# Optimization experiments

Hardware: AMD Instinct MI355X
Metric: run time of the kernel (lower is better)

The kernel has to match this reference:

```python
import jax, jax.numpy as jnp
import numpy as np

K = 8  # K_num: neighbors per pred point


def setup_inputs() -> dict:
    key = jax.random.key(0)
    ks = jax.random.split(key, 8)
    B, Nr, Np, C = 2, 8192, 8192, 256
    s = 1.0 / np.sqrt(C)
    return {
        "xyz_ref": jax.random.normal(ks[0], (B, Nr, 3), jnp.float32) * 10.0,
        "xyz_pred": jax.random.normal(ks[1], (B, Np, 3), jnp.float32) * 10.0,
        "feat_k_ref": jax.random.normal(ks[2], (B, Nr, C), jnp.float32),
        "feat_q_pred": jax.random.normal(ks[3], (B, Np, C), jnp.float32),
        "feat_v_ref": jax.random.normal(ks[4], (B, Nr, C), jnp.float32),
        "Wv": jax.random.normal(ks[5], (C, C), jnp.float32) * s,
        "bv": jnp.zeros((C,), jnp.float32),
        "Wo": jax.random.normal(ks[6], (C, C), jnp.float32) * s,
        "bo": jnp.zeros((C,), jnp.float32),
        "Wout": jax.random.normal(ks[7], (2 * C, C), jnp.float32) * s,
    }


def reference(xyz_ref, xyz_pred, feat_k_ref, feat_q_pred, feat_v_ref, Wv, bv, Wo, bo, Wout):
    B, Np, C = feat_q_pred.shape
    Nr = feat_k_ref.shape[1]

    # --- KNN search (torch.no_grad in original) ---
    xr = jax.lax.stop_gradient(xyz_ref)
    xp = jax.lax.stop_gradient(xyz_pred)
    d2 = (jnp.sum(xp * xp, -1)[:, :, None]
          + jnp.sum(xr * xr, -1)[:, None, :]
          - 2.0 * jnp.einsum('bpd,brd->bpr', xp, xr))  # [B, Np, Nr]
    _, idx = jax.lax.top_k(-d2, K)  # [B, Np, K] nearest ref indices per pred point

    # --- W_v (Conv1d 1x1) applied to all ref values before gather ---
    v_all = jnp.einsum('brc,dc->brd', feat_v_ref, Wv) + bv  # [B, Nr, C]

    gather = jax.vmap(lambda f, i: f[i])  # per-sample fancy gather
    k = gather(feat_k_ref, idx)  # [B, Np, K, C]
    v = gather(v_all, idx)       # [B, Np, K, C]

    # --- tiny per-point cross attention over K neighbors ---
    scores = jnp.einsum('bpc,bpkc->bpk', feat_q_pred, k) / jnp.sqrt(jnp.asarray(C, feat_q_pred.dtype))
    attn = jax.nn.softmax(scores, axis=-1)          # [B, Np, K]
    out = jnp.einsum('bpk,bpkc->bpc', attn, v)      # [B, Np, C]

    # --- W_o (Conv1d 1x1) ---
    out = jnp.einsum('bpc,dc->bpd', out, Wo) + bo   # [B, Np, C]

    # --- scatter into full point set: ref rows stay zero, pred rows get out ---
    out_all = jnp.concatenate([jnp.zeros((B, Nr, C), out.dtype), out], axis=1)  # [B, Nr+Np, C]

    # --- W_out (MinkowskiConvolution k=1, no bias): C -> 2C ---
    return jnp.einsum('bnc,dc->bnd', out_all, Wout)  # [B, Nr+Np, 2C]
```

## Files before the change

kernel.cpp:

```cpp
#include <hip/hip_runtime.h>
#include <stdint.h>


#define NRr 8192
#define NPp 8192
#define NC  256
#define NK  8
#define NCH   16
#define CHUNK 512

typedef short bf16x8 __attribute__((ext_vector_type(8)));
typedef float f32x4  __attribute__((ext_vector_type(4)));

__device__ __forceinline__ uint16_t f2bf(float f) {
  uint32_t u = __float_as_uint(f);
  return (uint16_t)((u + 0x7fffu + ((u >> 16) & 1u)) >> 16);
}

__device__ __forceinline__ float d2f(float px, float py, float pz, float sp, float4 r) {
  float m0 = __fmul_rn(px, r.x), m1 = __fmul_rn(py, r.y), m2 = __fmul_rn(pz, r.z);
  float dot = __fadd_rn(__fadd_rn(m0, m1), m2);
  return __fsub_rn(__fadd_rn(sp, r.w), __fadd_rn(dot, dot));
}

__device__ __forceinline__ uint32_t fkey(float f) {
  uint32_t b = __float_as_uint(f);
  return (b & 0x80000000u) ? ~b : (b | 0x80000000u);
}

__global__ __launch_bounds__(64) void k_prep(const float* __restrict__ xyz_ref,
                                             float4* __restrict__ ref4) {
  int i = blockIdx.x * 64 + threadIdx.x;
  if (i >= 2 * NRr) return;
  float x = xyz_ref[i*3+0];
  float y = xyz_ref[i*3+1];
  float z = xyz_ref[i*3+2];
  float n = __fadd_rn(__fadd_rn(__fmul_rn(x,x), __fmul_rn(y,y)), __fmul_rn(z,z));
  ref4[i] = make_float4(x, y, z, n);
}

__device__ __forceinline__ void insert8(float d2, int j, float (&dist)[8], int (&id)[8]) {
  if (d2 < dist[7]) {
    #pragma unroll
    for (int k = 7; k >= 1; --k) {
      bool sh = d2 < dist[k-1];
      bool pl = d2 < dist[k];
      float nd = sh ? dist[k-1] : (pl ? d2 : dist[k]);
      int   ni = sh ? id[k-1]   : (pl ? j  : id[k]);
      dist[k] = nd; id[k] = ni;
    }
    if (d2 < dist[0]) { dist[0] = d2; id[0] = j; }
  }
}

__global__ __launch_bounds__(256, 5) void k_knn(const float* __restrict__ xyz_pred,
                                                const float4* __restrict__ ref4,
                                                uint16_t* __restrict__ part,
                                                const float* __restrict__ Wv,
                                                const float* __restrict__ bv,
                                                const float* __restrict__ Wo,
                                                const float* __restrict__ bo,
                                                const float* __restrict__ Wout,
                                                uint16_t* __restrict__ Aw,
                                                float* __restrict__ bbig) {
  __shared__ __align__(16) char smem[32768];

  if (blockIdx.x < 64) {
    float (*M8)[256] = (float (*)[256])smem;
    float* red = (float*)(smem + 8192);
    int e0 = blockIdx.x * 8;
    int t  = threadIdx.x;

    float acc8[8];
    #pragma unroll
    for (int e = 0; e < 8; ++e) acc8[e] = 0.f;
    for (int d = 0; d < 256; ++d) {
      float wo = Wo[(size_t)d*256 + t];
      #pragma unroll
      for (int e = 0; e < 8; ++e)
        acc8[e] = fmaf(Wout[(size_t)(e0+e)*256 + d], wo, acc8[e]);
    }
    #pragma unroll
    for (int e = 0; e < 8; ++e) M8[e][t] = acc8[e];
    __syncthreads();

    float a8[8];
    #pragma unroll
    for (int e = 0; e < 8; ++e) a8[e] = 0.f;
    for (int c = 0; c < 256; ++c) {
      float wv = Wv[(size_t)c*256 + t];
      #pragma unroll
      for (int e = 0; e < 8; ++e)
        a8[e] = fmaf(M8[e][c], wv, a8[e]);
    }
    #pragma unroll
    for (int e = 0; e < 8; ++e) Aw[(size_t)(e0+e)*256 + t] = f2bf(a8[e]);

    for (int e = 0; e < 8; ++e) {
      red[t] = fmaf(M8[e][t], bv[t], Wout[(size_t)(e0+e)*256 + t] * bo[t]);
      __syncthreads();
      for (int s2 = 128; s2 > 0; s2 >>= 1) {
        if (t < s2) red[t] += red[t + s2];
        __syncthreads();
      }
      if (t == 0) bbig[e0+e] = red[0];
      __syncthreads();
    }
    return;
  }

  float4* sref = (float4*)smem;
  int wave = threadIdx.x >> 6;
  int lane = threadIdx.x & 63;
  int task = (blockIdx.x - 64) * 4 + wave;
  int ch   = task & (NCH - 1);
  int P    = (task >> 4) * 64 + lane;
  int b    = P >> 13;

  float px = xyz_pred[P*3+0];
  float py = xyz_pred[P*3+1];
  float pz = xyz_pred[P*3+2];
  float sp = __fadd_rn(__fadd_rn(__fmul_rn(px,px), __fmul_rn(py,py)), __fmul_rn(pz,pz));

  const float4* refbase = ref4 + (size_t)b * NRr;
  int rbase = ch * CHUNK;
  float4* srefw = sref + wave * CHUNK;
  for (int j = lane; j < CHUNK; j += 64) srefw[j] = refbase[rbase + j];

  float a0 = 3.4e38f, a1 = 3.4e38f, a2 = 3.4e38f, a3 = 3.4e38f;
  float g0 = 3.4e38f, g1 = 3.4e38f, g2 = 3.4e38f, g3 = 3.4e38f;
  float dist[8]; int id[8];
  #pragma unroll
  for (int k = 0; k < 8; ++k) { dist[k] = 3.4e38f; id[k] = 0; }

  for (int s = 0; s < CHUNK / 32; ++s) {
    uint32_t mm = 0;
    int base = s * 32;
    #pragma unroll 2
    for (int jj = 0; jj < 32; jj += 2) {
      float d0 = d2f(px, py, pz, sp, srefw[base + jj]);
      float d1 = d2f(px, py, pz, sp, srefw[base + jj + 1]);
      a3 = __builtin_amdgcn_fmed3f(d0, a2, a3);
      a2 = __builtin_amdgcn_fmed3f(d0, a1, a2);
      a1 = __builtin_amdgcn_fmed3f(d0, a0, a1);
      a0 = fminf(d0, a0);
      g3 = __builtin_amdgcn_fmed3f(d1, g2, g3);
      g2 = __builtin_amdgcn_fmed3f(d1, g1, g2);
      g1 = __builtin_amdgcn_fmed3f(d1, g0, g1);
      g0 = fminf(d1, g0);
      float tau = fmaxf(a3, g3);
      mm |= (uint32_t)(d0 <= tau) << jj;
      mm |= (uint32_t)(d1 <= tau) << (jj + 1);
    }
    while (mm) {
      int bit = __builtin_ctz(mm); mm &= mm - 1;
      int j = base + bit;
      float dd = d2f(px, py, pz, sp, srefw[j]);
      insert8(dd, j, dist, id);
    }
  }

  uint16_t* pp = part + ((size_t)P * NCH + ch) * 8;
  #pragma unroll
  for (int k = 0; k < 8; ++k)
    pp[k] = (uint16_t)((rbase + id[k]) & (NRr - 1));
}

__global__ __launch_bounds__(256) void k_attn(const float* __restrict__ feat_q,
    const float* __restrict__ feat_k, const float* __restrict__ feat_v,
    const uint16_t* __restrict__ part, const float* __restrict__ xyz_pred,
    const float4* __restrict__ ref4, uint16_t* __restrict__ g) {
  int wave = threadIdx.x >> 6;
  int lane = threadIdx.x & 63;
  int P = blockIdx.x * 4 + wave;
  int b = P >> 13;

  float px = xyz_pred[P*3+0];
  float py = xyz_pred[P*3+1];
  float pz = xyz_pred[P*3+2];
  float sp = __fadd_rn(__fadd_rn(__fmul_rn(px,px), __fmul_rn(py,py)), __fmul_rn(pz,pz));
  const float4* refbase = ref4 + (size_t)b * NRr;

  const uint32_t* pw = (const uint32_t*)(part + (size_t)P * (NCH * 8));
  uint32_t two = pw[lane];
  int j0 = two & (NRr - 1);
  int j1 = (two >> 16) & (NRr - 1);
  float d0 = d2f(px, py, pz, sp, refbase[j0]);
  float d1 = d2f(px, py, pz, sp, refbase[j1]);
  uint64_t k0 = ((uint64_t)fkey(d0) << 32) | (uint32_t)j0;
  uint64_t k1 = ((uint64_t)fkey(d1) << 32) | (uint32_t)j1;

  int nb[8];
  #pragma unroll
  for (int r = 0; r < 8; ++r) {
    uint64_t m = (k0 < k1) ? k0 : k1;
    #pragma unroll
    for (int s = 1; s < 64; s <<= 1) {
      uint64_t o = __shfl_xor(m, s, 64);
      m = (o < m) ? o : m;
    }
    nb[r] = (int)(uint32_t)(m & 0xFFFFFFFFu) & (NRr - 1);
    if (k0 == m) k0 = ~0ULL;
    if (k1 == m) k1 = ~0ULL;
  }

  float4 qv = *(const float4*)(feat_q + (size_t)P*NC + lane*4);
  const float* kb = feat_k + (size_t)b * NRr * NC;
  const float* vb = feat_v + (size_t)b * NRr * NC;

  float s[8];
  #pragma unroll
  for (int k = 0; k < 8; ++k) {
    float4 kv = *(const float4*)(kb + (size_t)nb[k]*NC + lane*4);
    float p = qv.x * kv.x;
    p = fmaf(qv.y, kv.y, p);
    p = fmaf(qv.z, kv.z, p);
    p = fmaf(qv.w, kv.w, p);
    s[k] = p;
  }
  #pragma unroll
  for (int k = 0; k < 8; ++k) {
    float v = s[k];
    #pragma unroll
    for (int m = 1; m < 64; m <<= 1) v += __shfl_xor(v, m, 64);
    s[k] = v * 0.0625f;
  }
  float mx = s[0];
  #pragma unroll
  for (int k = 1; k < 8; ++k) mx = fmaxf(mx, s[k]);
  float e[8], sum = 0.f;
  #pragma unroll
  for (int k = 0; k < 8; ++k) { e[k] = expf(s[k] - mx); sum += e[k]; }
  float inv = 1.0f / sum;

  float g0 = 0.f, g1 = 0.f, g2 = 0.f, g3 = 0.f;
  #pragma unroll
  for (int k = 0; k < 8; ++k) {
    float4 vv = *(const float4*)(vb + (size_t)nb[k]*NC + lane*4);
    float w = e[k] * inv;
    g0 = fmaf(w, vv.x, g0);
    g1 = fmaf(w, vv.y, g1);
    g2 = fmaf(w, vv.z, g2);
    g3 = fmaf(w, vv.w, g3);
  }
  uint32_t p0 = ((uint32_t)f2bf(g1) << 16) | f2bf(g0);
  uint32_t p1 = ((uint32_t)f2bf(g3) << 16) | f2bf(g2);
  *(uint2*)(g + (size_t)P*NC + lane*4) = make_uint2(p0, p1);
}

__global__ void k_zero(float4* __restrict__ o) {
  int i = blockIdx.x * 256 + threadIdx.x;
  int b = i >> 20;
  int r = i & 1048575;
  o[(size_t)b * 2097152 + r] = make_float4(0.f, 0.f, 0.f, 0.f);
}

__global__ __launch_bounds__(256) void k_gemm(const uint16_t* __restrict__ g,
    const uint16_t* __restrict__ Aw, const float* __restrict__ bbig,
    float* __restrict__ outp) {
  __shared__ __align__(16) uint16_t sA[64 * 136];
  __shared__ __align__(16) uint16_t sB[64 * 136];
  int t = threadIdx.x;
  int lane = t & 63, wave = t >> 6;
  int wm = (wave >> 1) * 32, wn = (wave & 1) * 32;
  int q = lane >> 4, rr = lane & 15;
  int bm = blockIdx.x;
  int bn = blockIdx.y;
  f32x4 zero = {0.f, 0.f, 0.f, 0.f};
  f32x4 acc[2][2] = {{zero, zero}, {zero, zero}};

  for (int ph = 0; ph < 2; ++ph) {
    #pragma unroll
    for (int i = 0; i < 4; ++i) {
      int cc  = t + i * 256;
      int row = cc >> 4;
      int col = (cc & 15) << 3;
      uint4 da = *(const uint4*)(g  + ((size_t)(bm*64 + row))*NC + ph*128 + col);
      *(uint4*)(&sA[row*136 + col]) = da;
      uint4 db = *(const uint4*)(Aw + ((size_t)(bn*64 + row))*NC + ph*128 + col);
      *(uint4*)(&sB[row*136 + col]) = db;
    }
    __syncthreads();
    #pragma unroll
    for (int kk = 0; kk < 4; ++kk) {
      int ko = kk*32 + q*8;
      bf16x8 a0 = *(const bf16x8*)(&sA[(wm      + rr)*136 + ko]);
      bf16x8 a1 = *(const bf16x8*)(&sA[(wm + 16 + rr)*136 + ko]);
      bf16x8 b0 = *(const bf16x8*)(&sB[(wn      + rr)*136 + ko]);
      bf16x8 b1 = *(const bf16x8*)(&sB[(wn + 16 + rr)*136 + ko]);
      acc[0][0] = __builtin_amdgcn_mfma_f32_16x16x32_bf16(a0, b0, acc[0][0], 0, 0, 0);
      acc[0][1] = __builtin_amdgcn_mfma_f32_16x16x32_bf16(a0, b1, acc[0][1], 0, 0, 0);
      acc[1][0] = __builtin_amdgcn_mfma_f32_16x16x32_bf16(a1, b0, acc[1][0], 0, 0, 0);
      acc[1][1] = __builtin_amdgcn_mfma_f32_16x16x32_bf16(a1, b1, acc[1][1], 0, 0, 0);
    }
    __syncthreads();
  }
  #pragma unroll
  for (int j = 0; j < 2; ++j) {
    int col = bn*64 + wn + j*16 + rr;
    float bias = bbig[col];
    #pragma unroll
    for (int i = 0; i < 2; ++i) {
      #pragma unroll
      for (int r = 0; r < 4; ++r) {
        int row = bm*64 + wm + i*16 + q*4 + r;
        float v = acc[i][j][r] + bias;
        int bb = row >> 13, p = row & 8191;
        outp[((size_t)(bb*16384 + 8192 + p))*512 + col] = v;
      }
    }
  }
}

extern "C" void kernel_launch(void* const* d_in, const int* in_sizes, int n_in,
                              void* d_out, int out_size, void* d_ws, size_t ws_size,
                              hipStream_t stream) {
  const float* xyz_ref  = (const float*)d_in[0];
  const float* xyz_pred = (const float*)d_in[1];
  const float* feat_k   = (const float*)d_in[2];
  const float* feat_q   = (const float*)d_in[3];
  const float* feat_v   = (const float*)d_in[4];
  const float* Wv       = (const float*)d_in[5];
  const float* bv       = (const float*)d_in[6];
  const float* Wo       = (const float*)d_in[7];
  const float* bo       = (const float*)d_in[8];
  const float* Wout     = (const float*)d_in[9];
  float* outp = (float*)d_out;

  char* ob = (char*)d_out;
  uint16_t* g    = (uint16_t*)ob;
  float4*   ref4 = (float4*)(ob + 8388608);
  uint16_t* Aw   = (uint16_t*)(ob + 9175040);
  float*    bbig = (float*)(ob + 9437184);
  uint16_t* part = (uint16_t*)(ob + 33554432);

  k_prep   <<<256,  64,  0, stream>>>(xyz_ref, ref4);
  k_knn    <<<1088, 256, 0, stream>>>(xyz_pred, ref4, part,
                                      Wv, bv, Wo, bo, Wout, Aw, bbig);
  k_attn   <<<4096, 256, 0, stream>>>(feat_q, feat_k, feat_v, part,
                                      xyz_pred, ref4, g);
  k_gemm   <<<dim3(256, 8), 256, 0, stream>>>(g, Aw, bbig, outp);
  k_zero   <<<8192, 256, 0, stream>>>((float4*)outp);
}
```

Measured before the change: 292.3 us.

## Split output zero-fill across prep, gemm and final zero kernels

The zero-fill of the reference rows of the output is split into pieces. Regions not used as scratch are cleared by extra blocks in k_prep, the region freed after attention is cleared by an extra column of blocks in k_gemm, and only the scratch regions used by g/ref4 remain for the final k_zero. This overlaps most of the zeroing with other kernels and shrinks the serial tail kernel, at the cost of intricate hardcoded offset arithmetic that must exactly avoid live scratch buffers.

```diff
diff --git a/kernel.cpp b/kernel.cpp
--- a/kernel.cpp
+++ b/kernel.cpp
@@ -29,7 +29,20 @@
 }
 
 __global__ __launch_bounds__(64) void k_prep(const float* __restrict__ xyz_ref,
-                                             float4* __restrict__ ref4) {
+                                             float4* __restrict__ ref4,
+                                             float4* __restrict__ ob4) {
+  if (blockIdx.x >= 256) {
+    int z = (blockIdx.x - 256) * 64 + threadIdx.x;
+    float4 zf = make_float4(0.f, 0.f, 0.f, 0.f);
+    for (int i = z; i < 1277824; i += 61440) {
+      size_t f;
+      if (i < 32768)       f = 540672u + i;
+      else if (i < 491392) f = 589952u + (i - 32768);
+      else                 f = 2359296u + (i - 491392);
+      ob4[f] = zf;
+    }
+    return;
+  }
   int i = blockIdx.x * 64 + threadIdx.x;
   if (i >= 2 * NRr) return;
   float x = xyz_ref[i*3+0];
@@ -249,10 +262,12 @@
 }
 
 __global__ void k_zero(float4* __restrict__ o) {
-  int i = blockIdx.x * 256 + threadIdx.x;
-  int b = i >> 20;
-  int r = i & 1048575;
-  o[(size_t)b * 2097152 + r] = make_float4(0.f, 0.f, 0.f, 0.f);
+  int z = blockIdx.x * 256 + threadIdx.x;
+  float4 zf = make_float4(0.f, 0.f, 0.f, 0.f);
+  for (int i = z; i < 540800; i += 524288) {
+    size_t f = (i < 524288) ? (size_t)i : (size_t)(573440 + (i - 524288));
+    o[f] = zf;
+  }
 }
 
 __global__ __launch_bounds__(256) void k_gemm(const uint16_t* __restrict__ g,
@@ -260,12 +275,23 @@
     float* __restrict__ outp) {
   __shared__ __align__(16) uint16_t sA[64 * 136];
   __shared__ __align__(16) uint16_t sB[64 * 136];
+  int bm = blockIdx.x;
+  int bn = blockIdx.y;
+  if (bm == 256) {
+    int z = bn * 256 + threadIdx.x;
+    float4 zf = make_float4(0.f, 0.f, 0.f, 0.f);
+    float4* o4 = (float4*)outp;
+    for (int i = z; i < 278528; i += 2048) {
+      size_t f = (i < 16384) ? (size_t)(524288 + i)
+                             : (size_t)(2097152 + (i - 16384));
+      o4[f] = zf;
+    }
+    return;
+  }
   int t = threadIdx.x;
   int lane = t & 63, wave = t >> 6;
   int wm = (wave >> 1) * 32, wn = (wave & 1) * 32;
   int q = lane >> 4, rr = lane & 15;
-  int bm = blockIdx.x;
-  int bn = blockIdx.y;
   f32x4 zero = {0.f, 0.f, 0.f, 0.f};
   f32x4 acc[2][2] = {{zero, zero}, {zero, zero}};
 
@@ -334,11 +360,11 @@
   float*    bbig = (float*)(ob + 9437184);
   uint16_t* part = (uint16_t*)(ob + 33554432);
 
-  k_prep   <<<256,  64,  0, stream>>>(xyz_ref, ref4);
+  k_prep   <<<1216, 64,  0, stream>>>(xyz_ref, ref4, (float4*)outp);
   k_knn    <<<1088, 256, 0, stream>>>(xyz_pred, ref4, part,
                                       Wv, bv, Wo, bo, Wout, Aw, bbig);
   k_attn   <<<4096, 256, 0, stream>>>(feat_q, feat_k, feat_v, part,
                                       xyz_pred, ref4, g);
-  k_gemm   <<<dim3(256, 8), 256, 0, stream>>>(g, Aw, bbig, outp);
-  k_zero   <<<8192, 256, 0, stream>>>((float4*)outp);
-}
+  k_gemm   <<<dim3(257, 8), 256, 0, stream>>>(g, Aw, bbig, outp);
+  k_zero   <<<2048, 256, 0, stream>>>((float4*)outp);
+}
```

Measured after the change: 301.3 us. +3.1%, slower.
